# Optimization experiments

Measured on AMD Instinct MI355X. Metric: run time of the kernel, lower is better.

## Reference

```python
import jax, jax.numpy as jnp
import numpy as np

TAU_FF = 10
TAU_FB = 10
NB_FF = 8
NB_FB = 1
MU = 0.5
N_IN = 2048
N_HID = 2048
N_OUT = 2048


def raised_cosine_pillow_08(tau, n_basis, mu):
    # Pillow et al. 2008 log-raised-cosine basis; returns [n_basis, tau].
    # Fixed (non-learned) constant in the original module.
    t = jnp.arange(tau, dtype=jnp.float32)
    c = jnp.arange(n_basis, dtype=jnp.float32)
    arg = jnp.clip(mu * jnp.pi * jnp.log1p(t)[None, :] - mu * jnp.pi * c[:, None],
                   -jnp.pi, jnp.pi)
    return 0.5 * (1.0 + jnp.cos(arg))


# transposed like the torch module: [tau, n_basis]
FF_FILT = raised_cosine_pillow_08(TAU_FF, NB_FF, MU).T
FB_FILT = raised_cosine_pillow_08(TAU_FB, NB_FB, MU).T


def _layer_step(inp_hist, spk_hist, ff_w, fb_w, bias, key):
    # inp_hist: [n_in, T]; spk_hist: [n_out, Th]; ff_w: [n_out, n_in, NB_FF]
    T = inp_hist.shape[-1]
    ff_trace = jnp.matmul(inp_hist[..., ::-1], FF_FILT[:T])       # [n_in, NB_FF]
    ff_pot = jnp.einsum('oib,ib->o', ff_w, ff_trace)              # [n_out]
    Th = spk_hist.shape[-1]
    fb_trace = jnp.matmul(spk_hist[:, ::-1], FB_FILT[:Th])        # [n_out, NB_FB]
    fb_pot = jnp.sum(fb_w * fb_trace, axis=-1)                    # [n_out]
    p = jax.nn.sigmoid(ff_pot + fb_pot + bias)
    spikes = jax.random.bernoulli(key, jax.lax.stop_gradient(p)).astype(p.dtype)
    # memory_length (10) > current history width (2), so the update just
    # appends one column (matches torch slice [:, 1-memory_length:]).
    new_hist = jnp.concatenate([spk_hist, spikes[:, None]], axis=-1)
    return p, spikes, new_hist


def setup_inputs() -> dict:
    key = jax.random.key(0)
    ks = jax.random.split(key, 10)

    def xav(k, shape, fan_in, fan_out):
        a = np.sqrt(3.0) * np.sqrt(2.0 / float(fan_in + fan_out))
        return jax.random.uniform(k, shape, jnp.float32, -a, a)

    fi, fo = N_IN * NB_FF, N_HID * NB_FF  # fan of ff_weights [n_out, n_in, nb]
    return {
        'inputs_history': (jax.random.uniform(ks[0], (N_IN, TAU_FF)) < 0.3).astype(jnp.float32),
        'ff_w0': xav(ks[1], (N_HID, N_IN, NB_FF), fi, fo),
        'fb_w0': xav(ks[2], (N_HID, NB_FB), fi, fo),
        'b0': xav(ks[3], (N_HID,), fi, fo),
        'ff_w1': xav(ks[4], (N_HID, N_HID, NB_FF), fi, fo),
        'fb_w1': xav(ks[5], (N_HID, NB_FB), fi, fo),
        'b1': xav(ks[6], (N_HID,), fi, fo),
        'ff_w2': xav(ks[7], (N_OUT, N_HID, NB_FF), fi, fo),
        'fb_w2': xav(ks[8], (N_OUT, NB_FB), fi, fo),
        'b2': xav(ks[9], (N_OUT,), fi, fo),
    }


def reference(inputs_history, ff_w0, fb_w0, b0, ff_w1, fb_w1, b1,
              ff_w2, fb_w2, b2):
    # LayeredSNN.forward with n_samples=1, target=None.
    k0, k1, k2 = jax.random.split(jax.random.key(42), 3)
    h0 = jnp.zeros((N_HID, 2), jnp.float32)   # initial spiking histories
    h1 = jnp.zeros((N_HID, 2), jnp.float32)
    h2 = jnp.zeros((N_OUT, 2), jnp.float32)
    p0, s0, h0 = _layer_step(inputs_history, h0, ff_w0, fb_w0, b0, k0)
    p1, s1, h1 = _layer_step(h0, h1, ff_w1, fb_w1, b1, k1)   # reads updated h0
    p2, s2, h2 = _layer_step(h1, h2, ff_w2, fb_w2, b2, k2)   # out layer
    net_probas = p2[None]                      # [1, n_out]
    net_outputs = s2[None]                     # [1, n_out]
    probas_hidden = jnp.stack([p0, p1])[None]  # [1, n_hidden_layers, n_hid]
    outputs_hidden = jnp.stack([s0, s1])[None]
    return net_probas, net_outputs, probas_hidden, outputs_hidden
```

## Files before the change

kernel.cpp:

```cpp
#include <hip/hip_runtime.h>
#include <hip/hip_bf16.h>
#include <stdint.h>
#include <stddef.h>

#define WS_F_OFF      64
#define WS_TRACE0_OFF 768
#define WS_S0_OFF     131840
#define WS_S1_OFF     148224

__host__ __device__ inline void tf2x32(uint32_t k0, uint32_t k1,
                                       uint32_t& x0, uint32_t& x1) {
  uint32_t ks0 = k0, ks1 = k1, ks2 = k0 ^ k1 ^ 0x1BD11BDAu;
  x0 += ks0; x1 += ks1;
#define TF_ROT(v, n) (((v) << (n)) | ((v) >> (32 - (n))))
#define TF_R(r) { x0 += x1; x1 = TF_ROT(x1, r); x1 ^= x0; }
  TF_R(13) TF_R(15) TF_R(26) TF_R(6)   x0 += ks1; x1 += ks2 + 1u;
  TF_R(17) TF_R(29) TF_R(16) TF_R(24)  x0 += ks2; x1 += ks0 + 2u;
  TF_R(13) TF_R(15) TF_R(26) TF_R(6)   x0 += ks0; x1 += ks1 + 3u;
  TF_R(17) TF_R(29) TF_R(16) TF_R(24)  x0 += ks1; x1 += ks2 + 4u;
  TF_R(13) TF_R(15) TF_R(26) TF_R(6)   x0 += ks2; x1 += ks0 + 5u;
#undef TF_R
#undef TF_ROT
}

__device__ inline double bf2d(unsigned short b) {
  return (double)__uint_as_float(((uint32_t)b) << 16);
}
__device__ inline unsigned short f2bf(float f) {
  uint32_t u = __float_as_uint(f);
  u += 0x7FFFu + ((u >> 16) & 1u);
  return (unsigned short)(u >> 16);
}

__global__ __launch_bounds__(256) void snn_prep_kernel(
    const void* __restrict__ X, uint8_t* __restrict__ ws) {
  __shared__ unsigned long long smask[4];
  __shared__ double sF[80];
  __shared__ int s_flag;
  const int tid = threadIdx.x;

  const uint32_t* xw = (const uint32_t*)X;
  uint32_t w = xw[tid];
  bool ok = (w == 0u || w == 0x3F800000u);
  unsigned long long m = __ballot(ok);
  if ((tid & 63) == 0) smask[tid >> 6] = m;

  if (tid < 80) {
    int tt = tid >> 3, b = tid & 7;
    const double PI = 3.14159265358979311599796346854;
    double arg = 0.5 * PI * log1p((double)tt) - 0.5 * PI * (double)b;
    arg = fmin(fmax(arg, -PI), PI);
    sF[tid] = 0.5 * (1.0 + cos(arg));
  }
  __syncthreads();
  if (tid == 0) {
    bool allbin = ((smask[0] & smask[1] & smask[2] & smask[3]) == ~0ull);
    s_flag = allbin ? 0 : 1;
  }
  __syncthreads();
  const int flag = s_flag;

  if (blockIdx.x == 0) {
    if (tid == 0) *(uint32_t*)ws = (uint32_t)flag;
    if (tid < 80) ((double*)(ws + WS_F_OFF))[tid] = sF[tid];
  }

  const int idx = blockIdx.x * 256 + tid;
  const int i = idx >> 3, b = idx & 7;
  double acc = 0.0;
  if (flag) {
    const unsigned short* Xb = (const unsigned short*)X;
    #pragma unroll
    for (int t = 0; t < 10; ++t) acc += bf2d(Xb[i * 10 + (9 - t)]) * sF[t * 8 + b];
  } else {
    const float* Xf = (const float*)X;
    #pragma unroll
    for (int t = 0; t < 10; ++t) acc += (double)Xf[i * 10 + (9 - t)] * sF[t * 8 + b];
  }
  ((double*)(ws + WS_TRACE0_OFF))[b * 2048 + i] = acc;
}

__global__ __launch_bounds__(256) void snn_layer_kernel(
    const void* __restrict__ W, const void* __restrict__ bias,
    const uint8_t* __restrict__ ws,
    int traceMode,
    const double* __restrict__ sPrev,
    double* __restrict__ sOutD,
    uint32_t key0, uint32_t key1,
    void* __restrict__ out, int pOff, int sOff)
{
  const uint32_t flag = *(const uint32_t*)ws;
  const double* F = (const double*)(ws + WS_F_OFF);
  const double* trT = (const double*)(ws + WS_TRACE0_OFF);
  const int lane = threadIdx.x & 63;
  const int wid  = threadIdx.x >> 6;
  const int row  = blockIdx.x * 2 + (wid >> 1);
  const int half = wid & 1;
  const int ibase = half * 1024;

  double acc[8];
  #pragma unroll
  for (int b = 0; b < 8; ++b) acc[b] = 0.0;

  if (traceMode == 0) {
    if (flag) {
      const unsigned short* Wr = (const unsigned short*)W + (size_t)row * 16384;
      #pragma unroll 4
      for (int s = 0; s < 16; ++s) {
        int i = ibase + s * 64 + lane;
        uint4 v = *(const uint4*)(Wr + i * 8);
        acc[0] += bf2d((unsigned short)(v.x & 0xFFFFu)) * trT[0 * 2048 + i];
        acc[1] += bf2d((unsigned short)(v.x >> 16))     * trT[1 * 2048 + i];
        acc[2] += bf2d((unsigned short)(v.y & 0xFFFFu)) * trT[2 * 2048 + i];
        acc[3] += bf2d((unsigned short)(v.y >> 16))     * trT[3 * 2048 + i];
        acc[4] += bf2d((unsigned short)(v.z & 0xFFFFu)) * trT[4 * 2048 + i];
        acc[5] += bf2d((unsigned short)(v.z >> 16))     * trT[5 * 2048 + i];
        acc[6] += bf2d((unsigned short)(v.w & 0xFFFFu)) * trT[6 * 2048 + i];
        acc[7] += bf2d((unsigned short)(v.w >> 16))     * trT[7 * 2048 + i];
      }
    } else {
      const float* Wr = (const float*)W + (size_t)row * 16384;
      #pragma unroll 4
      for (int s = 0; s < 16; ++s) {
        int i = ibase + s * 64 + lane;
        float4 a = *(const float4*)(Wr + i * 8);
        float4 c = *(const float4*)(Wr + i * 8 + 4);
        acc[0] += (double)a.x * trT[0 * 2048 + i];
        acc[1] += (double)a.y * trT[1 * 2048 + i];
        acc[2] += (double)a.z * trT[2 * 2048 + i];
        acc[3] += (double)a.w * trT[3 * 2048 + i];
        acc[4] += (double)c.x * trT[4 * 2048 + i];
        acc[5] += (double)c.y * trT[5 * 2048 + i];
        acc[6] += (double)c.z * trT[6 * 2048 + i];
        acc[7] += (double)c.w * trT[7 * 2048 + i];
      }
    }
  } else {
    double F0[8];
    #pragma unroll
    for (int b = 0; b < 8; ++b) F0[b] = F[b];
    if (flag) {
      const unsigned short* Wr = (const unsigned short*)W + (size_t)row * 16384;
      #pragma unroll 4
      for (int s = 0; s < 16; ++s) {
        int i = ibase + s * 64 + lane;
        uint4 v = *(const uint4*)(Wr + i * 8);
        double si = sPrev[i];
        acc[0] += (bf2d((unsigned short)(v.x & 0xFFFFu)) * F0[0]) * si;
        acc[1] += (bf2d((unsigned short)(v.x >> 16))     * F0[1]) * si;
        acc[2] += (bf2d((unsigned short)(v.y & 0xFFFFu)) * F0[2]) * si;
        acc[3] += (bf2d((unsigned short)(v.y >> 16))     * F0[3]) * si;
        acc[4] += (bf2d((unsigned short)(v.z & 0xFFFFu)) * F0[4]) * si;
        acc[5] += (bf2d((unsigned short)(v.z >> 16))     * F0[5]) * si;
        acc[6] += (bf2d((unsigned short)(v.w & 0xFFFFu)) * F0[6]) * si;
        acc[7] += (bf2d((unsigned short)(v.w >> 16))     * F0[7]) * si;
      }
    } else {
      const float* Wr = (const float*)W + (size_t)row * 16384;
      #pragma unroll 4
      for (int s = 0; s < 16; ++s) {
        int i = ibase + s * 64 + lane;
        float4 a = *(const float4*)(Wr + i * 8);
        float4 c = *(const float4*)(Wr + i * 8 + 4);
        double si = sPrev[i];
        acc[0] += ((double)a.x * F0[0]) * si;
        acc[1] += ((double)a.y * F0[1]) * si;
        acc[2] += ((double)a.z * F0[2]) * si;
        acc[3] += ((double)a.w * F0[3]) * si;
        acc[4] += ((double)c.x * F0[4]) * si;
        acc[5] += ((double)c.y * F0[5]) * si;
        acc[6] += ((double)c.z * F0[6]) * si;
        acc[7] += ((double)c.w * F0[7]) * si;
      }
    }
  }

  double r = ((acc[0] + acc[1]) + (acc[2] + acc[3])) +
             ((acc[4] + acc[5]) + (acc[6] + acc[7]));
  #pragma unroll
  for (int off = 32; off > 0; off >>= 1) r += __shfl_down(r, off, 64);

  __shared__ double sred[4];
  if (lane == 0) sred[wid] = r;
  __syncthreads();

  if (threadIdx.x < 2) {
    const int o = blockIdx.x * 2 + threadIdx.x;
    double rr = sred[2 * threadIdx.x] + sred[2 * threadIdx.x + 1];
    double bb = flag ? bf2d(((const unsigned short*)bias)[o])
                     : (double)((const float*)bias)[o];
    double x = rr + bb;
    double p = 1.0 / (1.0 + exp(-x));
    uint32_t x0 = 0u, x1 = (uint32_t)o;
    tf2x32(key0, key1, x0, x1);
    uint32_t wbits = x0 ^ x1;
    float u = __uint_as_float((wbits >> 9) | 0x3F800000u) - 1.0f;
    double sp = ((double)u < p) ? 1.0 : 0.0;
    if (flag) {
      unsigned short* ob = (unsigned short*)out;
      ob[pOff + o] = f2bf((float)p);
      ob[sOff + o] = f2bf((float)sp);
    } else {
      float* of = (float*)out;
      of[pOff + o] = (float)p;
      of[sOff + o] = (float)sp;
    }
    if (sOutD) sOutD[o] = sp;
  }
}

extern "C" void kernel_launch(void* const* d_in, const int* in_sizes, int n_in,
                              void* d_out, int out_size, void* d_ws, size_t ws_size,
                              hipStream_t stream) {
  uint32_t k0a = 0u, k0b = 0u;  tf2x32(0u, 42u, k0a, k0b);
  uint32_t k1a = 0u, k1b = 1u;  tf2x32(0u, 42u, k1a, k1b);
  uint32_t k2a = 0u, k2b = 2u;  tf2x32(0u, 42u, k2a, k2b);

  uint8_t* ws = (uint8_t*)d_ws;
  double* s0d = (double*)(ws + WS_S0_OFF);
  double* s1d = (double*)(ws + WS_S1_OFF);

  snn_prep_kernel<<<64, 256, 0, stream>>>(d_in[0], ws);
  snn_layer_kernel<<<1024, 256, 0, stream>>>(d_in[1], d_in[3], ws, 0, nullptr, s0d,
                                             k0a, k0b, d_out, 4096, 8192);
  snn_layer_kernel<<<1024, 256, 0, stream>>>(d_in[4], d_in[6], ws, 1, s0d, s1d,
                                             k1a, k1b, d_out, 6144, 10240);
  snn_layer_kernel<<<1024, 256, 0, stream>>>(d_in[7], d_in[9], ws, 1, s1d, nullptr,
                                             k2a, k2b, d_out, 0, 2048);
}
```

Baseline: 371.3 us.

## Use one block per output row with fully coalesced weight loads and interleaved trace

Each block now handles a single output row, and each wave takes a contiguous quarter of it. All of that wave's weight vectors are loaded up front into registers, with lanes reading consecutive 16-byte chunks so loads coalesce. The trace buffer is stored input-major ([i][b]) so each lane's 8 basis values sit together. Grid size doubles to 2048 blocks to issue more independent loads at once and raise memory-level parallelism, at the cost of more registers per thread and more block-level reductions.

```diff
diff --git a/kernel.cpp b/kernel.cpp
--- a/kernel.cpp
+++ b/kernel.cpp
@@ -77,7 +77,7 @@
     #pragma unroll
     for (int t = 0; t < 10; ++t) acc += (double)Xf[i * 10 + (9 - t)] * sF[t * 8 + b];
   }
-  ((double*)(ws + WS_TRACE0_OFF))[b * 2048 + i] = acc;
+  ((double*)(ws + WS_TRACE0_OFF))[idx] = acc;
 }
 
 __global__ __launch_bounds__(256) void snn_layer_kernel(
@@ -91,61 +91,45 @@
 {
   const uint32_t flag = *(const uint32_t*)ws;
   const double* F = (const double*)(ws + WS_F_OFF);
-  const double* trT = (const double*)(ws + WS_TRACE0_OFF);
+  const double* trI = (const double*)(ws + WS_TRACE0_OFF);
   const int lane = threadIdx.x & 63;
   const int wid  = threadIdx.x >> 6;
-  const int row  = blockIdx.x * 2 + (wid >> 1);
-  const int half = wid & 1;
-  const int ibase = half * 1024;
+  const int row  = blockIdx.x;
 
   double acc[8];
   #pragma unroll
   for (int b = 0; b < 8; ++b) acc[b] = 0.0;
 
-  if (traceMode == 0) {
-    if (flag) {
-      const unsigned short* Wr = (const unsigned short*)W + (size_t)row * 16384;
-      #pragma unroll 4
-      for (int s = 0; s < 16; ++s) {
-        int i = ibase + s * 64 + lane;
-        uint4 v = *(const uint4*)(Wr + i * 8);
-        acc[0] += bf2d((unsigned short)(v.x & 0xFFFFu)) * trT[0 * 2048 + i];
-        acc[1] += bf2d((unsigned short)(v.x >> 16))     * trT[1 * 2048 + i];
-        acc[2] += bf2d((unsigned short)(v.y & 0xFFFFu)) * trT[2 * 2048 + i];
-        acc[3] += bf2d((unsigned short)(v.y >> 16))     * trT[3 * 2048 + i];
-        acc[4] += bf2d((unsigned short)(v.z & 0xFFFFu)) * trT[4 * 2048 + i];
-        acc[5] += bf2d((unsigned short)(v.z >> 16))     * trT[5 * 2048 + i];
-        acc[6] += bf2d((unsigned short)(v.w & 0xFFFFu)) * trT[6 * 2048 + i];
-        acc[7] += bf2d((unsigned short)(v.w >> 16))     * trT[7 * 2048 + i];
+  if (flag) {
+    const uint4* Wq = (const uint4*)W + (size_t)row * 2048 + wid * 512;
+    uint4 wb[8];
+    #pragma unroll
+    for (int s = 0; s < 8; ++s) wb[s] = Wq[s * 64 + lane];
+
+    if (traceMode == 0) {
+      #pragma unroll
+      for (int s = 0; s < 8; ++s) {
+        int i = wid * 512 + s * 64 + lane;
+        const double* t = trI + (size_t)i * 8;
+        uint4 v = wb[s];
+        acc[0] += bf2d((unsigned short)(v.x & 0xFFFFu)) * t[0];
+        acc[1] += bf2d((unsigned short)(v.x >> 16))     * t[1];
+        acc[2] += bf2d((unsigned short)(v.y & 0xFFFFu)) * t[2];
+        acc[3] += bf2d((unsigned short)(v.y >> 16))     * t[3];
+        acc[4] += bf2d((unsigned short)(v.z & 0xFFFFu)) * t[4];
+        acc[5] += bf2d((unsigned short)(v.z >> 16))     * t[5];
+        acc[6] += bf2d((unsigned short)(v.w & 0xFFFFu)) * t[6];
+        acc[7] += bf2d((unsigned short)(v.w >> 16))     * t[7];
       }
     } else {
-      const float* Wr = (const float*)W + (size_t)row * 16384;
-      #pragma unroll 4
-      for (int s = 0; s < 16; ++s) {
-        int i = ibase + s * 64 + lane;
-        float4 a = *(const float4*)(Wr + i * 8);
-        float4 c = *(const float4*)(Wr + i * 8 + 4);
-        acc[0] += (double)a.x * trT[0 * 2048 + i];
-        acc[1] += (double)a.y * trT[1 * 2048 + i];
-        acc[2] += (double)a.z * trT[2 * 2048 + i];
-        acc[3] += (double)a.w * trT[3 * 2048 + i];
-        acc[4] += (double)c.x * trT[4 * 2048 + i];
-        acc[5] += (double)c.y * trT[5 * 2048 + i];
-        acc[6] += (double)c.z * trT[6 * 2048 + i];
-        acc[7] += (double)c.w * trT[7 * 2048 + i];
-      }
-    }
-  } else {
-    double F0[8];
-    #pragma unroll
-    for (int b = 0; b < 8; ++b) F0[b] = F[b];
-    if (flag) {
-      const unsigned short* Wr = (const unsigned short*)W + (size_t)row * 16384;
-      #pragma unroll 4
-      for (int s = 0; s < 16; ++s) {
-        int i = ibase + s * 64 + lane;
-        uint4 v = *(const uint4*)(Wr + i * 8);
+      double F0[8];
+      #pragma unroll
+      for (int b = 0; b < 8; ++b) F0[b] = F[b];
+      #pragma unroll
+      for (int s = 0; s < 8; ++s) {
+        int i = wid * 512 + s * 64 + lane;
         double si = sPrev[i];
+        uint4 v = wb[s];
         acc[0] += (bf2d((unsigned short)(v.x & 0xFFFFu)) * F0[0]) * si;
         acc[1] += (bf2d((unsigned short)(v.x >> 16))     * F0[1]) * si;
         acc[2] += (bf2d((unsigned short)(v.y & 0xFFFFu)) * F0[2]) * si;
@@ -155,22 +139,56 @@
         acc[6] += (bf2d((unsigned short)(v.w & 0xFFFFu)) * F0[6]) * si;
         acc[7] += (bf2d((unsigned short)(v.w >> 16))     * F0[7]) * si;
       }
+    }
+  } else {
+    const int ebase = wid * 1024;
+    const float4* Wq = (const float4*)W + (size_t)row * 4096 + ebase;
+    float4 wv[16];
+    #pragma unroll
+    for (int s = 0; s < 8; ++s) {
+      wv[2 * s]     = Wq[s * 128 + lane];
+      wv[2 * s + 1] = Wq[s * 128 + 64 + lane];
+    }
+
+    if (traceMode == 0) {
+      #pragma unroll
+      for (int s = 0; s < 8; ++s) {
+        int e0 = ebase + s * 128 + lane;
+        int e1 = e0 + 64;
+        const double* t0 = trI + (size_t)e0 * 4;
+        const double* t1 = trI + (size_t)e1 * 4;
+        float4 a = wv[2 * s];
+        float4 c = wv[2 * s + 1];
+        acc[0] += (double)a.x * t0[0];
+        acc[1] += (double)a.y * t0[1];
+        acc[2] += (double)a.z * t0[2];
+        acc[3] += (double)a.w * t0[3];
+        acc[4] += (double)c.x * t1[0];
+        acc[5] += (double)c.y * t1[1];
+        acc[6] += (double)c.z * t1[2];
+        acc[7] += (double)c.w * t1[3];
+      }
     } else {
-      const float* Wr = (const float*)W + (size_t)row * 16384;
-      #pragma unroll 4
-      for (int s = 0; s < 16; ++s) {
-        int i = ibase + s * 64 + lane;
-        float4 a = *(const float4*)(Wr + i * 8);
-        float4 c = *(const float4*)(Wr + i * 8 + 4);
-        double si = sPrev[i];
-        acc[0] += ((double)a.x * F0[0]) * si;
-        acc[1] += ((double)a.y * F0[1]) * si;
-        acc[2] += ((double)a.z * F0[2]) * si;
-        acc[3] += ((double)a.w * F0[3]) * si;
-        acc[4] += ((double)c.x * F0[4]) * si;
-        acc[5] += ((double)c.y * F0[5]) * si;
-        acc[6] += ((double)c.z * F0[6]) * si;
-        acc[7] += ((double)c.w * F0[7]) * si;
+      double F0[4];
+      const int p = lane & 1;
+      #pragma unroll
+      for (int j = 0; j < 4; ++j) F0[j] = F[p * 4 + j];
+      #pragma unroll
+      for (int s = 0; s < 8; ++s) {
+        int e0 = ebase + s * 128 + lane;
+        int e1 = e0 + 64;
+        double s0v = sPrev[e0 >> 1];
+        double s1v = sPrev[e1 >> 1];
+        float4 a = wv[2 * s];
+        float4 c = wv[2 * s + 1];
+        acc[0] += ((double)a.x * F0[0]) * s0v;
+        acc[1] += ((double)a.y * F0[1]) * s0v;
+        acc[2] += ((double)a.z * F0[2]) * s0v;
+        acc[3] += ((double)a.w * F0[3]) * s0v;
+        acc[4] += ((double)c.x * F0[0]) * s1v;
+        acc[5] += ((double)c.y * F0[1]) * s1v;
+        acc[6] += ((double)c.z * F0[2]) * s1v;
+        acc[7] += ((double)c.w * F0[3]) * s1v;
       }
     }
   }
@@ -184,9 +202,9 @@
   if (lane == 0) sred[wid] = r;
   __syncthreads();
 
-  if (threadIdx.x < 2) {
-    const int o = blockIdx.x * 2 + threadIdx.x;
-    double rr = sred[2 * threadIdx.x] + sred[2 * threadIdx.x + 1];
+  if (threadIdx.x == 0) {
+    const int o = blockIdx.x;
+    double rr = (sred[0] + sred[1]) + (sred[2] + sred[3]);
     double bb = flag ? bf2d(((const unsigned short*)bias)[o])
                      : (double)((const float*)bias)[o];
     double x = rr + bb;
@@ -221,10 +239,10 @@
   double* s1d = (double*)(ws + WS_S1_OFF);
 
   snn_prep_kernel<<<64, 256, 0, stream>>>(d_in[0], ws);
-  snn_layer_kernel<<<1024, 256, 0, stream>>>(d_in[1], d_in[3], ws, 0, nullptr, s0d,
+  snn_layer_kernel<<<2048, 256, 0, stream>>>(d_in[1], d_in[3], ws, 0, nullptr, s0d,
                                              k0a, k0b, d_out, 4096, 8192);
-  snn_layer_kernel<<<1024, 256, 0, stream>>>(d_in[4], d_in[6], ws, 1, s0d, s1d,
+  snn_layer_kernel<<<2048, 256, 0, stream>>>(d_in[4], d_in[6], ws, 1, s0d, s1d,
                                              k1a, k1b, d_out, 6144, 10240);
-  snn_layer_kernel<<<1024, 256, 0, stream>>>(d_in[7], d_in[9], ws, 1, s1d, nullptr,
+  snn_layer_kernel<<<2048, 256, 0, stream>>>(d_in[7], d_in[9], ws, 1, s1d, nullptr,
                                              k2a, k2b, d_out, 0, 2048);
 }
```

New measurement: 378.2 us. About the same (+1.9%).

## Fuse prep and three layer kernels into one cooperative launch with grid syncs

Applied to the files above, without the earlier changes.

Merges the prep kernel and the three layer kernels into a single cooperative kernel that separates stages with grid-wide syncs and thread fences. This is meant to remove per-launch overhead and the gaps between kernels. The occupancy hint is set to 4 blocks per CU so that all 1024 blocks can be resident. If the cooperative launch fails, the code falls back to the original four separate launches. In exchange it adds grid-sync cost and may lower occupancy or raise register use in the fused kernel.

```diff
diff --git a/kernel.cpp b/kernel.cpp
--- a/kernel.cpp
+++ b/kernel.cpp
@@ -1,7 +1,9 @@
 #include <hip/hip_runtime.h>
-#include <hip/hip_bf16.h>
+#include <hip/hip_cooperative_groups.h>
 #include <stdint.h>
 #include <stddef.h>
+
+namespace cg = cooperative_groups;
 
 #define WS_F_OFF      64
 #define WS_TRACE0_OFF 768
@@ -32,8 +34,7 @@
   return (unsigned short)(u >> 16);
 }
 
-__global__ __launch_bounds__(256) void snn_prep_kernel(
-    const void* __restrict__ X, uint8_t* __restrict__ ws) {
+__device__ void prep_body(const void* __restrict__ X, uint8_t* __restrict__ ws) {
   __shared__ unsigned long long smask[4];
   __shared__ double sF[80];
   __shared__ int s_flag;
@@ -80,7 +81,7 @@
   ((double*)(ws + WS_TRACE0_OFF))[b * 2048 + i] = acc;
 }
 
-__global__ __launch_bounds__(256) void snn_layer_kernel(
+__device__ void layer_body(
     const void* __restrict__ W, const void* __restrict__ bias,
     const uint8_t* __restrict__ ws,
     int traceMode,
@@ -207,6 +208,50 @@
     }
     if (sOutD) sOutD[o] = sp;
   }
+  __syncthreads();
+}
+
+__global__ __launch_bounds__(256, 4) void snn_fused(
+    const void* __restrict__ X,
+    const void* __restrict__ W0, const void* __restrict__ B0,
+    const void* __restrict__ W1, const void* __restrict__ B1,
+    const void* __restrict__ W2, const void* __restrict__ B2,
+    uint8_t* __restrict__ ws,
+    uint32_t k0a, uint32_t k0b, uint32_t k1a, uint32_t k1b,
+    uint32_t k2a, uint32_t k2b,
+    void* __restrict__ out)
+{
+  cg::grid_group grid = cg::this_grid();
+  double* s0d = (double*)(ws + WS_S0_OFF);
+  double* s1d = (double*)(ws + WS_S1_OFF);
+
+  if (blockIdx.x < 64) prep_body(X, ws);
+  __threadfence();
+  grid.sync();
+
+  layer_body(W0, B0, ws, 0, nullptr, s0d, k0a, k0b, out, 4096, 8192);
+  __threadfence();
+  grid.sync();
+
+  layer_body(W1, B1, ws, 1, s0d, s1d, k1a, k1b, out, 6144, 10240);
+  __threadfence();
+  grid.sync();
+
+  layer_body(W2, B2, ws, 1, s1d, nullptr, k2a, k2b, out, 0, 2048);
+}
+
+__global__ __launch_bounds__(256) void snn_prep_kernel(
+    const void* __restrict__ X, uint8_t* __restrict__ ws) {
+  prep_body(X, ws);
+}
+
+__global__ __launch_bounds__(256) void snn_layer_kernel(
+    const void* __restrict__ W, const void* __restrict__ bias,
+    const uint8_t* __restrict__ ws, int traceMode,
+    const double* __restrict__ sPrev, double* __restrict__ sOutD,
+    uint32_t key0, uint32_t key1,
+    void* __restrict__ out, int pOff, int sOff) {
+  layer_body(W, bias, ws, traceMode, sPrev, sOutD, key0, key1, out, pOff, sOff);
 }
 
 extern "C" void kernel_launch(void* const* d_in, const int* in_sizes, int n_in,
@@ -220,11 +265,28 @@
   double* s0d = (double*)(ws + WS_S0_OFF);
   double* s1d = (double*)(ws + WS_S1_OFF);
 
-  snn_prep_kernel<<<64, 256, 0, stream>>>(d_in[0], ws);
-  snn_layer_kernel<<<1024, 256, 0, stream>>>(d_in[1], d_in[3], ws, 0, nullptr, s0d,
-                                             k0a, k0b, d_out, 4096, 8192);
-  snn_layer_kernel<<<1024, 256, 0, stream>>>(d_in[4], d_in[6], ws, 1, s0d, s1d,
-                                             k1a, k1b, d_out, 6144, 10240);
-  snn_layer_kernel<<<1024, 256, 0, stream>>>(d_in[7], d_in[9], ws, 1, s1d, nullptr,
-                                             k2a, k2b, d_out, 0, 2048);
-}
+  const void* X  = d_in[0];
+  const void* W0 = d_in[1]; const void* B0 = d_in[3];
+  const void* W1 = d_in[4]; const void* B1 = d_in[6];
+  const void* W2 = d_in[7]; const void* B2 = d_in[9];
+  void* outp = d_out;
+
+  void* kargs[] = { (void*)&X, (void*)&W0, (void*)&B0, (void*)&W1, (void*)&B1,
+                    (void*)&W2, (void*)&B2, (void*)&ws,
+                    (void*)&k0a, (void*)&k0b, (void*)&k1a, (void*)&k1b,
+                    (void*)&k2a, (void*)&k2b, (void*)&outp };
+
+  hipError_t e = hipLaunchCooperativeKernel((const void*)snn_fused,
+                                            dim3(1024), dim3(256),
+                                            kargs, 0, stream);
+  if (e != hipSuccess) {
+    (void)hipGetLastError();
+    snn_prep_kernel<<<64, 256, 0, stream>>>(X, ws);
+    snn_layer_kernel<<<1024, 256, 0, stream>>>(W0, B0, ws, 0, nullptr, s0d,
+                                               k0a, k0b, d_out, 4096, 8192);
+    snn_layer_kernel<<<1024, 256, 0, stream>>>(W1, B1, ws, 1, s0d, s1d,
+                                               k1a, k1b, d_out, 6144, 10240);
+    snn_layer_kernel<<<1024, 256, 0, stream>>>(W2, B2, ws, 1, s1d, nullptr,
+                                               k2a, k2b, d_out, 0, 2048);
+  }
+}
```

Measured after the change: 978.7 us. +163.6%, slower.

## Split layers into per-column partial-sum kernel plus finalize kernel with coefficient tables

Applied to the files above, without the earlier changes.

Each layer is split into an accumulation kernel and a finalize kernel. In the accumulation kernel every wavefront keeps one 64-wide slice of input coefficients in registers and sweeps 16 output rows, writing one partial sum per row per slice. The finalize kernel reduces the 32 partials and applies bias, sigmoid and sampling. It also writes a unified [i,8] coefficient table (filter times spike) for the next layer, so all layers share one code path. This cuts the repeated strided trace loads and issues more independent weight loads per thread, at the cost of three extra launches, partial-buffer traffic and one wave reduction per row.

```diff
diff --git a/kernel.cpp b/kernel.cpp
--- a/kernel.cpp
+++ b/kernel.cpp
@@ -3,10 +3,11 @@
 #include <stdint.h>
 #include <stddef.h>
 
-#define WS_F_OFF      64
-#define WS_TRACE0_OFF 768
-#define WS_S0_OFF     131840
-#define WS_S1_OFF     148224
+#define WS_F_OFF   64
+#define WS_CT0     768
+#define WS_CT1     131840
+#define WS_CT2     262912
+#define WS_PART    394240
 
 __host__ __device__ inline void tf2x32(uint32_t k0, uint32_t k1,
                                        uint32_t& x0, uint32_t& x1) {
@@ -32,6 +33,12 @@
   return (unsigned short)(u >> 16);
 }
 
+__device__ inline double wred64(double r) {
+  #pragma unroll
+  for (int off = 32; off > 0; off >>= 1) r += __shfl_down(r, off, 64);
+  return r;
+}
+
 __global__ __launch_bounds__(256) void snn_prep_kernel(
     const void* __restrict__ X, uint8_t* __restrict__ ws) {
   __shared__ unsigned long long smask[4];
@@ -77,135 +84,123 @@
     #pragma unroll
     for (int t = 0; t < 10; ++t) acc += (double)Xf[i * 10 + (9 - t)] * sF[t * 8 + b];
   }
-  ((double*)(ws + WS_TRACE0_OFF))[b * 2048 + i] = acc;
-}
-
-__global__ __launch_bounds__(256) void snn_layer_kernel(
-    const void* __restrict__ W, const void* __restrict__ bias,
-    const uint8_t* __restrict__ ws,
-    int traceMode,
-    const double* __restrict__ sPrev,
-    double* __restrict__ sOutD,
+  ((double*)(ws + WS_CT0))[idx] = acc;
+}
+
+__global__ __launch_bounds__(256) void snn_acc_kernel(
+    const void* __restrict__ W, const uint8_t* __restrict__ ws,
+    const double* __restrict__ cTab, double* __restrict__ partial)
+{
+  const uint32_t flag = *(const uint32_t*)ws;
+  const int lane = threadIdx.x & 63;
+  const int wid  = threadIdx.x >> 6;
+  const int wg   = blockIdx.x * 4 + wid;
+  const int ig   = wg & 31;
+  const int rc   = wg >> 5;
+  const int i    = ig * 64 + lane;
+  const int row0 = rc * 16;
+
+  double c8[8];
+  {
+    const double* cp = cTab + (size_t)i * 8;
+    #pragma unroll
+    for (int b = 0; b < 8; ++b) c8[b] = cp[b];
+  }
+
+  if (flag) {
+    const unsigned short* base =
+        (const unsigned short*)W + (size_t)row0 * 16384 + (size_t)i * 8;
+    for (int rr = 0; rr < 16; rr += 4) {
+      uint4 v0 = *(const uint4*)(base + (size_t)(rr + 0) * 16384);
+      uint4 v1 = *(const uint4*)(base + (size_t)(rr + 1) * 16384);
+      uint4 v2 = *(const uint4*)(base + (size_t)(rr + 2) * 16384);
+      uint4 v3 = *(const uint4*)(base + (size_t)(rr + 3) * 16384);
+      #pragma unroll
+      for (int k = 0; k < 4; ++k) {
+        uint4 v = (k == 0) ? v0 : (k == 1) ? v1 : (k == 2) ? v2 : v3;
+        double t0 = bf2d((unsigned short)(v.x & 0xFFFFu)) * c8[0];
+        double t1 = bf2d((unsigned short)(v.x >> 16))     * c8[1];
+        double t2 = bf2d((unsigned short)(v.y & 0xFFFFu)) * c8[2];
+        double t3 = bf2d((unsigned short)(v.y >> 16))     * c8[3];
+        double t4 = bf2d((unsigned short)(v.z & 0xFFFFu)) * c8[4];
+        double t5 = bf2d((unsigned short)(v.z >> 16))     * c8[5];
+        double t6 = bf2d((unsigned short)(v.w & 0xFFFFu)) * c8[6];
+        double t7 = bf2d((unsigned short)(v.w >> 16))     * c8[7];
+        double r = ((t0 + t1) + (t2 + t3)) + ((t4 + t5) + (t6 + t7));
+        r = wred64(r);
+        if (lane == 0) partial[(size_t)ig * 2048 + row0 + rr + k] = r;
+      }
+    }
+  } else {
+    const float* base =
+        (const float*)W + (size_t)row0 * 16384 + (size_t)i * 8;
+    for (int rr = 0; rr < 16; rr += 4) {
+      float4 a0 = *(const float4*)(base + (size_t)(rr + 0) * 16384);
+      float4 c0 = *(const float4*)(base + (size_t)(rr + 0) * 16384 + 4);
+      float4 a1 = *(const float4*)(base + (size_t)(rr + 1) * 16384);
+      float4 c1 = *(const float4*)(base + (size_t)(rr + 1) * 16384 + 4);
+      float4 a2 = *(const float4*)(base + (size_t)(rr + 2) * 16384);
+      float4 c2 = *(const float4*)(base + (size_t)(rr + 2) * 16384 + 4);
+      float4 a3 = *(const float4*)(base + (size_t)(rr + 3) * 16384);
+      float4 c3 = *(const float4*)(base + (size_t)(rr + 3) * 16384 + 4);
+      #pragma unroll
+      for (int k = 0; k < 4; ++k) {
+        float4 a = (k == 0) ? a0 : (k == 1) ? a1 : (k == 2) ? a2 : a3;
+        float4 c = (k == 0) ? c0 : (k == 1) ? c1 : (k == 2) ? c2 : c3;
+        double t0 = (double)a.x * c8[0];
+        double t1 = (double)a.y * c8[1];
+        double t2 = (double)a.z * c8[2];
+        double t3 = (double)a.w * c8[3];
+        double t4 = (double)c.x * c8[4];
+        double t5 = (double)c.y * c8[5];
+        double t6 = (double)c.z * c8[6];
+        double t7 = (double)c.w * c8[7];
+        double r = ((t0 + t1) + (t2 + t3)) + ((t4 + t5) + (t6 + t7));
+        r = wred64(r);
+        if (lane == 0) partial[(size_t)ig * 2048 + row0 + rr + k] = r;
+      }
+    }
+  }
+}
+
+__global__ __launch_bounds__(256) void snn_fin_kernel(
+    const uint8_t* __restrict__ ws, const double* __restrict__ partial,
+    const void* __restrict__ bias,
+    double* __restrict__ cNext,
     uint32_t key0, uint32_t key1,
     void* __restrict__ out, int pOff, int sOff)
 {
   const uint32_t flag = *(const uint32_t*)ws;
   const double* F = (const double*)(ws + WS_F_OFF);
-  const double* trT = (const double*)(ws + WS_TRACE0_OFF);
-  const int lane = threadIdx.x & 63;
-  const int wid  = threadIdx.x >> 6;
-  const int row  = blockIdx.x * 2 + (wid >> 1);
-  const int half = wid & 1;
-  const int ibase = half * 1024;
-
-  double acc[8];
-  #pragma unroll
-  for (int b = 0; b < 8; ++b) acc[b] = 0.0;
-
-  if (traceMode == 0) {
-    if (flag) {
-      const unsigned short* Wr = (const unsigned short*)W + (size_t)row * 16384;
-      #pragma unroll 4
-      for (int s = 0; s < 16; ++s) {
-        int i = ibase + s * 64 + lane;
-        uint4 v = *(const uint4*)(Wr + i * 8);
-        acc[0] += bf2d((unsigned short)(v.x & 0xFFFFu)) * trT[0 * 2048 + i];
-        acc[1] += bf2d((unsigned short)(v.x >> 16))     * trT[1 * 2048 + i];
-        acc[2] += bf2d((unsigned short)(v.y & 0xFFFFu)) * trT[2 * 2048 + i];
-        acc[3] += bf2d((unsigned short)(v.y >> 16))     * trT[3 * 2048 + i];
-        acc[4] += bf2d((unsigned short)(v.z & 0xFFFFu)) * trT[4 * 2048 + i];
-        acc[5] += bf2d((unsigned short)(v.z >> 16))     * trT[5 * 2048 + i];
-        acc[6] += bf2d((unsigned short)(v.w & 0xFFFFu)) * trT[6 * 2048 + i];
-        acc[7] += bf2d((unsigned short)(v.w >> 16))     * trT[7 * 2048 + i];
-      }
-    } else {
-      const float* Wr = (const float*)W + (size_t)row * 16384;
-      #pragma unroll 4
-      for (int s = 0; s < 16; ++s) {
-        int i = ibase + s * 64 + lane;
-        float4 a = *(const float4*)(Wr + i * 8);
-        float4 c = *(const float4*)(Wr + i * 8 + 4);
-        acc[0] += (double)a.x * trT[0 * 2048 + i];
-        acc[1] += (double)a.y * trT[1 * 2048 + i];
-        acc[2] += (double)a.z * trT[2 * 2048 + i];
-        acc[3] += (double)a.w * trT[3 * 2048 + i];
-        acc[4] += (double)c.x * trT[4 * 2048 + i];
-        acc[5] += (double)c.y * trT[5 * 2048 + i];
-        acc[6] += (double)c.z * trT[6 * 2048 + i];
-        acc[7] += (double)c.w * trT[7 * 2048 + i];
-      }
-    }
+  const int o = blockIdx.x * 256 + threadIdx.x;
+
+  double r = 0.0;
+  #pragma unroll 8
+  for (int ig = 0; ig < 32; ++ig) r += partial[(size_t)ig * 2048 + o];
+
+  double bb = flag ? bf2d(((const unsigned short*)bias)[o])
+                   : (double)((const float*)bias)[o];
+  double x = r + bb;
+  double p = 1.0 / (1.0 + exp(-x));
+  uint32_t x0 = 0u, x1 = (uint32_t)o;
+  tf2x32(key0, key1, x0, x1);
+  uint32_t wbits = x0 ^ x1;
+  float u = __uint_as_float((wbits >> 9) | 0x3F800000u) - 1.0f;
+  double sp = ((double)u < p) ? 1.0 : 0.0;
+
+  if (flag) {
+    unsigned short* ob = (unsigned short*)out;
+    ob[pOff + o] = f2bf((float)p);
+    ob[sOff + o] = f2bf((float)sp);
   } else {
-    double F0[8];
-    #pragma unroll
-    for (int b = 0; b < 8; ++b) F0[b] = F[b];
-    if (flag) {
-      const unsigned short* Wr = (const unsigned short*)W + (size_t)row * 16384;
-      #pragma unroll 4
-      for (int s = 0; s < 16; ++s) {
-        int i = ibase + s * 64 + lane;
-        uint4 v = *(const uint4*)(Wr + i * 8);
-        double si = sPrev[i];
-        acc[0] += (bf2d((unsigned short)(v.x & 0xFFFFu)) * F0[0]) * si;
-        acc[1] += (bf2d((unsigned short)(v.x >> 16))     * F0[1]) * si;
-        acc[2] += (bf2d((unsigned short)(v.y & 0xFFFFu)) * F0[2]) * si;
-        acc[3] += (bf2d((unsigned short)(v.y >> 16))     * F0[3]) * si;
-        acc[4] += (bf2d((unsigned short)(v.z & 0xFFFFu)) * F0[4]) * si;
-        acc[5] += (bf2d((unsigned short)(v.z >> 16))     * F0[5]) * si;
-        acc[6] += (bf2d((unsigned short)(v.w & 0xFFFFu)) * F0[6]) * si;
-        acc[7] += (bf2d((unsigned short)(v.w >> 16))     * F0[7]) * si;
-      }
-    } else {
-      const float* Wr = (const float*)W + (size_t)row * 16384;
-      #pragma unroll 4
-      for (int s = 0; s < 16; ++s) {
-        int i = ibase + s * 64 + lane;
-        float4 a = *(const float4*)(Wr + i * 8);
-        float4 c = *(const float4*)(Wr + i * 8 + 4);
-        double si = sPrev[i];
-        acc[0] += ((double)a.x * F0[0]) * si;
-        acc[1] += ((double)a.y * F0[1]) * si;
-        acc[2] += ((double)a.z * F0[2]) * si;
-        acc[3] += ((double)a.w * F0[3]) * si;
-        acc[4] += ((double)c.x * F0[4]) * si;
-        acc[5] += ((double)c.y * F0[5]) * si;
-        acc[6] += ((double)c.z * F0[6]) * si;
-        acc[7] += ((double)c.w * F0[7]) * si;
-      }
-    }
-  }
-
-  double r = ((acc[0] + acc[1]) + (acc[2] + acc[3])) +
-             ((acc[4] + acc[5]) + (acc[6] + acc[7]));
-  #pragma unroll
-  for (int off = 32; off > 0; off >>= 1) r += __shfl_down(r, off, 64);
-
-  __shared__ double sred[4];
-  if (lane == 0) sred[wid] = r;
-  __syncthreads();
-
-  if (threadIdx.x < 2) {
-    const int o = blockIdx.x * 2 + threadIdx.x;
-    double rr = sred[2 * threadIdx.x] + sred[2 * threadIdx.x + 1];
-    double bb = flag ? bf2d(((const unsigned short*)bias)[o])
-                     : (double)((const float*)bias)[o];
-    double x = rr + bb;
-    double p = 1.0 / (1.0 + exp(-x));
-    uint32_t x0 = 0u, x1 = (uint32_t)o;
-    tf2x32(key0, key1, x0, x1);
-    uint32_t wbits = x0 ^ x1;
-    float u = __uint_as_float((wbits >> 9) | 0x3F800000u) - 1.0f;
-    double sp = ((double)u < p) ? 1.0 : 0.0;
-    if (flag) {
-      unsigned short* ob = (unsigned short*)out;
-      ob[pOff + o] = f2bf((float)p);
-      ob[sOff + o] = f2bf((float)sp);
-    } else {
-      float* of = (float*)out;
-      of[pOff + o] = (float)p;
-      of[sOff + o] = (float)sp;
-    }
-    if (sOutD) sOutD[o] = sp;
+    float* of = (float*)out;
+    of[pOff + o] = (float)p;
+    of[sOff + o] = (float)sp;
+  }
+  if (cNext) {
+    double* cp = cNext + (size_t)o * 8;
+    #pragma unroll
+    for (int b = 0; b < 8; ++b) cp[b] = F[b] * sp;
   }
 }
 
@@ -217,14 +212,25 @@
   uint32_t k2a = 0u, k2b = 2u;  tf2x32(0u, 42u, k2a, k2b);
 
   uint8_t* ws = (uint8_t*)d_ws;
-  double* s0d = (double*)(ws + WS_S0_OFF);
-  double* s1d = (double*)(ws + WS_S1_OFF);
-
-  snn_prep_kernel<<<64, 256, 0, stream>>>(d_in[0], ws);
-  snn_layer_kernel<<<1024, 256, 0, stream>>>(d_in[1], d_in[3], ws, 0, nullptr, s0d,
-                                             k0a, k0b, d_out, 4096, 8192);
-  snn_layer_kernel<<<1024, 256, 0, stream>>>(d_in[4], d_in[6], ws, 1, s0d, s1d,
-                                             k1a, k1b, d_out, 6144, 10240);
-  snn_layer_kernel<<<1024, 256, 0, stream>>>(d_in[7], d_in[9], ws, 1, s1d, nullptr,
-                                             k2a, k2b, d_out, 0, 2048);
-}
+  double* ct0  = (double*)(ws + WS_CT0);
+  double* ct1  = (double*)(ws + WS_CT1);
+  double* ct2  = (double*)(ws + WS_CT2);
+  double* part = (double*)(ws + WS_PART);
+
+  const void* X  = d_in[0];
+  const void* W0 = d_in[1]; const void* B0 = d_in[3];
+  const void* W1 = d_in[4]; const void* B1 = d_in[6];
+  const void* W2 = d_in[7]; const void* B2 = d_in[9];
+
+  snn_prep_kernel<<<64, 256, 0, stream>>>(X, ws);
+
+  snn_acc_kernel<<<1024, 256, 0, stream>>>(W0, ws, ct0, part);
+  snn_fin_kernel<<<8, 256, 0, stream>>>(ws, part, B0, ct1,
+                                        k0a, k0b, d_out, 4096, 8192);
+  snn_acc_kernel<<<1024, 256, 0, stream>>>(W1, ws, ct1, part);
+  snn_fin_kernel<<<8, 256, 0, stream>>>(ws, part, B1, ct2,
+                                        k1a, k1b, d_out, 6144, 10240);
+  snn_acc_kernel<<<1024, 256, 0, stream>>>(W2, ws, ct2, part);
+  snn_fin_kernel<<<8, 256, 0, stream>>>(ws, part, B2, nullptr,
+                                        k2a, k2b, d_out, 0, 2048);
+}
```

New measurement: 389.0 us. +4.8%, slower.
